# Kernel optimization log

Measured on AMD Instinct MI355X. Metric: run time of the kernel, lower is better.

Reference implementation:

```python
import jax, jax.numpy as jnp
import numpy as np

# module hyperparameters (init kwargs)
D_MODEL = 1024
NUM_HEADS = 16
D_K = D_MODEL // NUM_HEADS
WINDOW_SIZE = 256
GLOBAL_TOKENS = 64
SEQ_LEN = 4096
BATCH = 1
NEG_INF = float('-inf')


def build_local_window_mask(seq_len, window_size, global_tokens):
    # 0 where attention is allowed, -inf where blocked
    i = jnp.arange(seq_len)[:, None]
    j = jnp.arange(seq_len)[None, :]
    allowed = (i < global_tokens) | (j < global_tokens) | (jnp.abs(i - j) <= window_size)
    return jnp.where(allowed, 0.0, NEG_INF).astype(jnp.float32)


def setup_inputs() -> dict:
    key = jax.random.key(0)
    ks = jax.random.split(key, 12)
    s = 1.0 / np.sqrt(D_MODEL)
    inp = {
        'q': jax.random.normal(ks[0], (BATCH, SEQ_LEN, D_MODEL), jnp.float32),
        'k': jax.random.normal(ks[1], (BATCH, SEQ_LEN, D_MODEL), jnp.float32),
        'v': jax.random.normal(ks[2], (BATCH, SEQ_LEN, D_MODEL), jnp.float32),
        # nn.Linear weights: shape (out, in), applied as x @ W.T + b
        'w_q': jax.random.normal(ks[3], (D_MODEL, D_MODEL), jnp.float32) * s,
        'b_q': jax.random.normal(ks[4], (D_MODEL,), jnp.float32) * s,
        'w_k': jax.random.normal(ks[5], (D_MODEL, D_MODEL), jnp.float32) * s,
        'b_k': jax.random.normal(ks[6], (D_MODEL,), jnp.float32) * s,
        'w_v': jax.random.normal(ks[7], (D_MODEL, D_MODEL), jnp.float32) * s,
        'b_v': jax.random.normal(ks[8], (D_MODEL,), jnp.float32) * s,
        'w_o': jax.random.normal(ks[9], (D_MODEL, D_MODEL), jnp.float32) * s,
        'b_o': jax.random.normal(ks[10], (D_MODEL,), jnp.float32) * s,
    }
    return inp


def reference(q, k, v, w_q, b_q, w_k, b_k, w_v, b_v, w_o, b_o):
    B, S, _ = q.shape
    scale = 1.0 / np.sqrt(D_K)

    def proj(x, w, b):  # (B,S,D) -> (B,H,S,Dk)
        y = x @ w.T + b
        return y.reshape(B, S, NUM_HEADS, D_K).transpose(0, 2, 1, 3)

    Q = proj(q, w_q, b_q)
    K = proj(k, w_k, b_k)
    V = proj(v, w_v, b_v)

    local_mask = build_local_window_mask(S, WINDOW_SIZE, GLOBAL_TOKENS)  # (S,S)
    scores = jnp.einsum('bhqd,bhkd->bhqk', Q, K) * scale + local_mask[None, None]
    attn = jax.nn.softmax(scores, axis=-1)
    out = jnp.einsum('bhqk,bhkd->bhqd', attn, V)  # (B,H,S,Dk)
    out = out.transpose(0, 2, 1, 3).reshape(B, S, D_MODEL)
    return out @ w_o.T + b_o
```

## Files before the change

### kernel.cpp

```cpp
#include <hip/hip_runtime.h>

#define S_LEN 4096
#define DMODEL 1024
#define NHEADS 16
#define DKH 64
#define WIN 256
#define GTOK 64
#define NSPLIT 8

typedef unsigned short u16t;
typedef __attribute__((ext_vector_type(8))) short short8;
typedef __attribute__((ext_vector_type(4))) float f32x4;

__device__ __forceinline__ u16t f2bf(float x) {
  union { float f; unsigned int u; } v; v.f = x;
  unsigned int r = v.u + 0x7FFFu + ((v.u >> 16) & 1u);
  return (u16t)(r >> 16);
}

__device__ __forceinline__ unsigned int cvtpk(float lo, float hi) {
  unsigned int r;
  asm("v_cvt_pk_bf16_f32 %0, %1, %2" : "=v"(r) : "v"(lo), "v"(hi));
  return r;
}

__device__ __forceinline__ void gload_lds16(const u16t* g, u16t* l) {
  __builtin_amdgcn_global_load_lds(
      (const __attribute__((address_space(1))) void*)g,
      (__attribute__((address_space(3))) void*)l, 16, 0, 0);
}

__global__ void cvt_all(const float* __restrict__ s0, const float* __restrict__ s1,
                        const float* __restrict__ s2, const float* __restrict__ s3,
                        const float* __restrict__ s4, const float* __restrict__ s5,
                        const float* __restrict__ s6,
                        u16t* __restrict__ d0, u16t* __restrict__ d1,
                        u16t* __restrict__ d2, u16t* __restrict__ d3,
                        u16t* __restrict__ d4, u16t* __restrict__ d5,
                        u16t* __restrict__ d6) {
  size_t i = (size_t)blockIdx.x * 1024 + threadIdx.x * 4;
  const float* s; u16t* d; size_t local;
  if (i < ((size_t)4 << 20)) {
    int which = (int)(i >> 20);
    local = i & ((1u << 20) - 1);
    s = which == 0 ? s0 : which == 1 ? s1 : which == 2 ? s2 : s3;
    d = which == 0 ? d0 : which == 1 ? d1 : which == 2 ? d2 : d3;
  } else {
    size_t j = i - ((size_t)4 << 20);
    int which = (int)(j >> 22);
    local = j & ((1u << 22) - 1);
    s = which == 0 ? s4 : which == 1 ? s5 : s6;
    d = which == 0 ? d4 : which == 1 ? d5 : d6;
  }
  float4 f = *(const float4*)(s + local);
  unsigned int lo = (unsigned int)f2bf(f.x) | ((unsigned int)f2bf(f.y) << 16);
  unsigned int hi = (unsigned int)f2bf(f.z) | ((unsigned int)f2bf(f.w) << 16);
  *(uint2*)(d + local) = make_uint2(lo, hi);
}

#define BN 128
#define GBK 64

template<int OUT_F32, int BMT, int BIAS_ROW>
__device__ __forceinline__
void gemm_body(u16t* __restrict__ sA, u16t* __restrict__ sB,
               const u16t* __restrict__ A, const u16t* __restrict__ B,
               const float* __restrict__ bias, void* __restrict__ Y,
               int N, int K, float alpha, int m0, int n0)
{
  constexpr int MF = BMT / 32;
  constexpr int CA_ISS = BMT * 2 / 64;

  const int tid = threadIdx.x;
  const int lane = tid & 63;
  const int lr = lane & 15, lg = lane >> 4;
  const int w = tid >> 6;
  const int wm = (w >> 1) * (MF * 16), wn = (w & 1) * 64;

  f32x4 acc[MF][4] = {};
  const int nk = K / GBK;

  for (int kt = 0; kt < nk; ++kt) {
    if (kt) __syncthreads();
#pragma unroll
    for (int i = 0; i < CA_ISS; ++i) {
      int c0 = w * (BMT * 2) + i * 64;
      int c = c0 + lane;
      int row = c >> 3, g = (c & 7) ^ (row & 7);
      gload_lds16(A + (size_t)(m0 + row) * K + kt * GBK + g * 8, sA + (size_t)c0 * 8);
    }
#pragma unroll
    for (int i = 0; i < 4; ++i) {
      int c0 = w * 256 + i * 64;
      int c = c0 + lane;
      int row = c >> 3, g = (c & 7) ^ (row & 7);
      gload_lds16(B + (size_t)(n0 + row) * K + kt * GBK + g * 8, sB + (size_t)c0 * 8);
    }
    __syncthreads();

    short8 af[MF][2], bf[4][2];
#pragma unroll
    for (int mf = 0; mf < MF; ++mf)
#pragma unroll
      for (int kk = 0; kk < 2; ++kk) {
        int s = ((kk * 4 + lg) ^ (lr & 7));
        af[mf][kk] = *(const short8*)&sA[(wm + mf * 16 + lr) * GBK + s * 8];
      }
#pragma unroll
    for (int nf = 0; nf < 4; ++nf)
#pragma unroll
      for (int kk = 0; kk < 2; ++kk) {
        int s = ((kk * 4 + lg) ^ (lr & 7));
        bf[nf][kk] = *(const short8*)&sB[(wn + nf * 16 + lr) * GBK + s * 8];
      }
    __builtin_amdgcn_s_setprio(1);
#pragma unroll
    for (int kk = 0; kk < 2; ++kk)
#pragma unroll
      for (int mf = 0; mf < MF; ++mf)
#pragma unroll
        for (int nf = 0; nf < 4; ++nf)
          acc[mf][nf] = __builtin_amdgcn_mfma_f32_16x16x32_bf16(af[mf][kk], bf[nf][kk], acc[mf][nf], 0, 0, 0);
    __builtin_amdgcn_s_setprio(0);
  }

#pragma unroll
  for (int nf = 0; nf < 4; ++nf) {
    int col = n0 + wn + nf * 16 + lr;
    float bvc = BIAS_ROW ? 0.f : bias[col];
#pragma unroll
    for (int mf = 0; mf < MF; ++mf)
#pragma unroll
      for (int r = 0; r < 4; ++r) {
        int row = m0 + wm + mf * 16 + lg * 4 + r;
        float bv = BIAS_ROW ? bias[row] : bvc;
        float v = (acc[mf][nf][r] + bv) * alpha;
        if (OUT_F32) ((float*)Y)[(size_t)row * N + col] = v;
        else         ((u16t*)Y)[(size_t)row * N + col] = f2bf(v);
      }
  }
}

#define QSCALE 0.18033688011112042f
__global__ __launch_bounds__(256)
void gemm_qkv(const u16t* __restrict__ xq, const u16t* __restrict__ xk, const u16t* __restrict__ xv,
              const u16t* __restrict__ wq, const u16t* __restrict__ wk, const u16t* __restrict__ wv,
              const float* __restrict__ bq, const float* __restrict__ bk, const float* __restrict__ bv,
              u16t* __restrict__ Qp, u16t* __restrict__ Kp, u16t* __restrict__ Vt)
{
  __shared__ __align__(16) u16t smem[2 * 128 * GBK];
  u16t* sA = smem;
  u16t* sB = smem + 128 * GBK;

  int b = blockIdx.x;
  int wid = (b & 7) * 96 + (b >> 3);
  int z = wid >> 8;
  int rem = wid & 255;
  if (z == 0) {
    gemm_body<0, 128, 0>(sA, sB, xq, wq, bq, Qp, DMODEL, DMODEL, QSCALE, (rem >> 3) * 128, (rem & 7) * BN);
  } else if (z == 1) {
    gemm_body<0, 128, 0>(sA, sB, xk, wk, bk, Kp, DMODEL, DMODEL, 1.0f, (rem >> 3) * 128, (rem & 7) * BN);
  } else {
    gemm_body<0, 128, 1>(sA, sB, wv, xv, bv, Vt, S_LEN, DMODEL, 1.0f, (rem & 7) * 128, (rem >> 3) * BN);
  }
}

__global__ __launch_bounds__(256)
void gemm_o(const u16t* __restrict__ A, const u16t* __restrict__ B,
            const float* __restrict__ bias, float* __restrict__ Y)
{
  __shared__ __align__(16) u16t smem[(64 + 128) * GBK];
  u16t* sA = smem;
  u16t* sB = smem + 64 * GBK;

  int b = blockIdx.x;
  int wid = (b & 7) * 64 + (b >> 3);
  int my = wid >> 3, mx = wid & 7;
  gemm_body<1, 64, 0>(sA, sB, A, B, bias, Y, DMODEL, DMODEL, 1.0f, my * 64, mx * BN);
}

__global__ __launch_bounds__(256)
void attn_kernel(const u16t* __restrict__ Qp, const u16t* __restrict__ Kp,
                 const u16t* __restrict__ Vt, u16t* __restrict__ AO,
                 float* __restrict__ pacc, float* __restrict__ pml)
{
  __shared__ __align__(16) u16t sK[2][64 * 64];
  __shared__ __align__(16) u16t sV[2][64 * 64];
  __shared__ __align__(16) u16t sP[4][16 * 64];

  const int b = blockIdx.x;
  const int wid = (b & 7) * 142 + (b >> 3);
  const int h = wid / 71;
  const int x = wid % 71;

  const int tid = threadIdx.x, w = tid >> 6, lane = tid & 63;
  const int lr = lane & 15, lg = lane >> 4;

  const bool windowed = (x < 63);
  const int qb = windowed ? (x + 1) : 0;
  const int split = windowed ? 0 : (x - 63);
  const int qw = qb * 64 + w * 16;

  short8 qf[2];
#pragma unroll
  for (int kk = 0; kk < 2; ++kk)
    qf[kk] = *(const short8*)(Qp + (size_t)(qw + lr) * DMODEL + h * DKH + kk * 32 + lg * 8);

  f32x4 acc[4] = {};
  float m_run = -1e30f, l_run = 0.f;

  int lo = 1, nkv;
  if (windowed) {
    lo = (qb - 4 < 1) ? 1 : qb - 4;
    int hi = (qb + 4 > 63) ? 63 : qb + 4;
    nkv = hi - lo + 2;
  } else {
    nkv = 64 / NSPLIT;
  }

#define KVB(idx) (windowed ? ((idx) == 0 ? 0 : lo + (idx) - 1) : (split * (64 / NSPLIT) + (idx)))

  auto stage = [&](int buf, int kvb) {
    int kv0 = kvb * 64;
#pragma unroll
    for (int j = 0; j < 2; ++j) {
      int c = tid + j * 256;
      int row = c >> 3, g = (c & 7) ^ (row & 7);
      gload_lds16(Kp + (size_t)(kv0 + row) * DMODEL + h * DKH + g * 8, &sK[buf][c * 8]);
    }
#pragma unroll
    for (int j = 0; j < 2; ++j) {
      int c = tid + j * 256;
      int row = c >> 3, g = (c & 7) ^ (row & 7);
      gload_lds16(Vt + (size_t)(h * DKH + row) * S_LEN + kv0 + g * 8, &sV[buf][c * 8]);
    }
  };

  stage(0, KVB(0));
  __syncthreads();

  for (int idx = 0; idx < nkv; ++idx) {
    const int buf = idx & 1;
    const int kvb = KVB(idx);
    const int kv0 = kvb * 64;

    if (idx + 1 < nkv) stage(buf ^ 1, KVB(idx + 1));

    f32x4 sacc[4] = {};
    __builtin_amdgcn_s_setprio(1);
#pragma unroll
    for (int kk = 0; kk < 2; ++kk)
#pragma unroll
      for (int nf = 0; nf < 4; ++nf) {
        int s = ((kk * 4 + lg) ^ (lr & 7));
        short8 kf = *(const short8*)&sK[buf][(nf * 16 + lr) * 64 + s * 8];
        sacc[nf] = __builtin_amdgcn_mfma_f32_16x16x32_bf16(kf, qf[kk], sacc[nf], 0, 0, 0);
      }
    __builtin_amdgcn_s_setprio(0);

    if (windowed && (kvb == qb + 4 || (kvb == qb - 4 && kvb > 0))) {
      int qg = qw + lr;
#pragma unroll
      for (int nf = 0; nf < 4; ++nf)
#pragma unroll
        for (int r = 0; r < 4; ++r) {
          int sg = kv0 + nf * 16 + lg * 4 + r;
          int diff = qg - sg; if (diff < 0) diff = -diff;
          if (diff > WIN) sacc[nf][r] = -1e30f;
        }
    }

    float rm0 = fmaxf(fmaxf(sacc[0][0], sacc[0][1]), sacc[0][2]);
    float rm1 = fmaxf(fmaxf(sacc[0][3], sacc[1][0]), sacc[1][1]);
    float rm2 = fmaxf(fmaxf(sacc[1][2], sacc[1][3]), sacc[2][0]);
    float rm3 = fmaxf(fmaxf(sacc[2][1], sacc[2][2]), sacc[2][3]);
    float rm4 = fmaxf(fmaxf(sacc[3][0], sacc[3][1]), sacc[3][2]);
    float rm = fmaxf(fmaxf(rm0, rm1), fmaxf(fmaxf(rm2, rm3), fmaxf(rm4, sacc[3][3])));
    rm = fmaxf(rm, __shfl_xor(rm, 16));
    rm = fmaxf(rm, __shfl_xor(rm, 32));

    if (!__all(rm <= m_run + 11.0f)) {
      float mnew = fmaxf(m_run, rm);
      float corr = exp2f(m_run - mnew);
      m_run = mnew;
      l_run *= corr;
      float cq[4];
#pragma unroll
      for (int r = 0; r < 4; ++r) cq[r] = __shfl(corr, lg * 4 + r);
#pragma unroll
      for (int nf = 0; nf < 4; ++nf)
#pragma unroll
        for (int r = 0; r < 4; ++r) acc[nf][r] *= cq[r];
    }

    float p[4][4];
    float rs = 0.f;
#pragma unroll
    for (int nf = 0; nf < 4; ++nf)
#pragma unroll
      for (int r = 0; r < 4; ++r) {
        float e = exp2f(sacc[nf][r] - m_run);
        p[nf][r] = e;
        rs += e;
      }
    rs += __shfl_xor(rs, 16);
    rs += __shfl_xor(rs, 32);
    l_run += rs;

#pragma unroll
    for (int nf = 0; nf < 4; ++nf) {
      unsigned int lo32 = cvtpk(p[nf][0], p[nf][1]);
      unsigned int hi32 = cvtpk(p[nf][2], p[nf][3]);
      int blk = (nf * 2 + (lg >> 1)) ^ (lr & 7);
      *(uint2*)&sP[w][lr * 64 + blk * 8 + (lg & 1) * 4] = make_uint2(lo32, hi32);
    }

#pragma unroll
    for (int kk = 0; kk < 2; ++kk) {
      short8 pf = *(const short8*)&sP[w][lr * 64 + (((kk * 4 + lg) ^ (lr & 7))) * 8];
      __builtin_amdgcn_s_setprio(1);
#pragma unroll
      for (int nf = 0; nf < 4; ++nf) {
        int s = ((kk * 4 + lg) ^ (lr & 7));
        short8 vf = *(const short8*)&sV[buf][(nf * 16 + lr) * 64 + s * 8];
        acc[nf] = __builtin_amdgcn_mfma_f32_16x16x32_bf16(pf, vf, acc[nf], 0, 0, 0);
      }
      __builtin_amdgcn_s_setprio(0);
    }

    if (idx + 1 < nkv) __syncthreads();
  }
#undef KVB

  if (windowed) {
    float lq[4];
#pragma unroll
    for (int r = 0; r < 4; ++r) lq[r] = __shfl(l_run, lg * 4 + r);
#pragma unroll
    for (int nf = 0; nf < 4; ++nf)
#pragma unroll
      for (int r = 0; r < 4; ++r) {
        float v = acc[nf][r] / lq[r];
        AO[(size_t)(qw + lg * 4 + r) * DMODEL + h * DKH + nf * 16 + lr] = f2bf(v);
      }
  } else {
    const int pbase = (h * NSPLIT + split) * 64;
#pragma unroll
    for (int nf = 0; nf < 4; ++nf)
#pragma unroll
      for (int r = 0; r < 4; ++r)
        pacc[(size_t)(pbase + w * 16 + lg * 4 + r) * 64 + nf * 16 + lr] = acc[nf][r];
    if (lane < 16) {
      int bb = (pbase + w * 16 + lane) * 2;
      pml[bb] = m_run;
      pml[bb + 1] = l_run;
    }
  }
}

__global__ __launch_bounds__(256)
void merge_kernel(const float* __restrict__ pacc, const float* __restrict__ pml,
                  u16t* __restrict__ AO)
{
  const int h = blockIdx.x;
  const int tid = threadIdx.x;
  const int row = tid >> 2;
  const int d0 = (tid & 3) * 16;

  float M = -1e30f;
#pragma unroll
  for (int s = 0; s < NSPLIT; ++s)
    M = fmaxf(M, pml[((h * NSPLIT + s) * 64 + row) * 2]);

  float L = 0.f;
  float o[16];
#pragma unroll
  for (int e = 0; e < 16; ++e) o[e] = 0.f;

#pragma unroll
  for (int s = 0; s < NSPLIT; ++s) {
    int b = ((h * NSPLIT + s) * 64 + row) * 2;
    float sc = exp2f(pml[b] - M);
    L += pml[b + 1] * sc;
    const float4* a = (const float4*)(pacc + ((size_t)(h * NSPLIT + s) * 64 + row) * 64 + d0);
#pragma unroll
    for (int q4 = 0; q4 < 4; ++q4) {
      float4 av = a[q4];
      o[q4 * 4 + 0] += av.x * sc;
      o[q4 * 4 + 1] += av.y * sc;
      o[q4 * 4 + 2] += av.z * sc;
      o[q4 * 4 + 3] += av.w * sc;
    }
  }
  float inv = 1.f / L;
#pragma unroll
  for (int e = 0; e < 16; ++e)
    AO[(size_t)row * DMODEL + h * DKH + d0 + e] = f2bf(o[e] * inv);
}

extern "C" void kernel_launch(void* const* d_in, const int* in_sizes, int n_in,
                              void* d_out, int out_size, void* d_ws, size_t ws_size,
                              hipStream_t stream) {
  const float* q   = (const float*)d_in[0];
  const float* k   = (const float*)d_in[1];
  const float* v   = (const float*)d_in[2];
  const float* w_q = (const float*)d_in[3];
  const float* b_q = (const float*)d_in[4];
  const float* w_k = (const float*)d_in[5];
  const float* b_k = (const float*)d_in[6];
  const float* w_v = (const float*)d_in[7];
  const float* b_v = (const float*)d_in[8];
  const float* w_o = (const float*)d_in[9];
  const float* b_o = (const float*)d_in[10];

  u16t* ws = (u16t*)d_ws;
  const size_t SZX = (size_t)S_LEN * DMODEL;
  const size_t SZW = (size_t)DMODEL * DMODEL;
  u16t* xq  = ws;
  u16t* xk  = xq + SZX;
  u16t* xv  = xk + SZX;
  u16t* wb0 = xv + SZX;
  u16t* wb1 = wb0 + SZW;
  u16t* wb2 = wb1 + SZW;
  u16t* wb3 = wb2 + SZW;
  u16t* Qp  = wb3 + SZW;
  u16t* Kp  = Qp + SZX;
  u16t* Vt  = Kp + SZX;
  u16t* AO  = xk;
  float* pacc = (float*)xq;
  float* pml  = pacc + (size_t)NHEADS * NSPLIT * 64 * 64;

  dim3 blk(256);

  cvt_all<<<(int)((4 * SZW + 3 * SZX) / 1024), blk, 0, stream>>>(
      w_q, w_k, w_v, w_o, q, k, v, wb0, wb1, wb2, wb3, xq, xk, xv);

  gemm_qkv<<<768, blk, 0, stream>>>(xq, xk, xv, wb0, wb1, wb2, b_q, b_k, b_v, Qp, Kp, Vt);

  attn_kernel<<<(63 + NSPLIT) * NHEADS, blk, 0, stream>>>(Qp, Kp, Vt, AO, pacc, pml);
  merge_kernel<<<NHEADS, blk, 0, stream>>>(pacc, pml, AO);

  gemm_o<<<512, blk, 0, stream>>>(AO, wb3, b_o, (float*)d_out);
}
```

Baseline: 113.8 us.

## Load K/V fragments directly from global memory into registers in attention

Removes the double-buffered LDS staging of K and V tiles and the per-iteration block barriers. Each wave now loads its own MFMA K and V operand fragments straight from global memory into registers. This drops LDS traffic and synchronisation, but all four waves in a block now fetch the same K/V data redundantly. Load latency is also no longer hidden by prefetching the next tile, so it relies on L2/cache hits and on occupancy.

```diff
diff --git a/kernel.cpp b/kernel.cpp
--- a/kernel.cpp
+++ b/kernel.cpp
@@ -184,8 +184,6 @@
                  const u16t* __restrict__ Vt, u16t* __restrict__ AO,
                  float* __restrict__ pacc, float* __restrict__ pml)
 {
-  __shared__ __align__(16) u16t sK[2][64 * 64];
-  __shared__ __align__(16) u16t sV[2][64 * 64];
   __shared__ __align__(16) u16t sP[4][16 * 64];
 
   const int b = blockIdx.x;
@@ -218,45 +216,41 @@
     nkv = 64 / NSPLIT;
   }
 
+  const u16t* Kl = Kp + h * DKH + (size_t)lr * DMODEL + lg * 8;
+  const u16t* Vl = Vt + (size_t)(h * DKH + lr) * S_LEN + lg * 8;
+
 #define KVB(idx) (windowed ? ((idx) == 0 ? 0 : lo + (idx) - 1) : (split * (64 / NSPLIT) + (idx)))
 
-  auto stage = [&](int buf, int kvb) {
-    int kv0 = kvb * 64;
-#pragma unroll
-    for (int j = 0; j < 2; ++j) {
-      int c = tid + j * 256;
-      int row = c >> 3, g = (c & 7) ^ (row & 7);
-      gload_lds16(Kp + (size_t)(kv0 + row) * DMODEL + h * DKH + g * 8, &sK[buf][c * 8]);
-    }
-#pragma unroll
-    for (int j = 0; j < 2; ++j) {
-      int c = tid + j * 256;
-      int row = c >> 3, g = (c & 7) ^ (row & 7);
-      gload_lds16(Vt + (size_t)(h * DKH + row) * S_LEN + kv0 + g * 8, &sV[buf][c * 8]);
-    }
-  };
-
-  stage(0, KVB(0));
-  __syncthreads();
-
   for (int idx = 0; idx < nkv; ++idx) {
-    const int buf = idx & 1;
     const int kvb = KVB(idx);
     const int kv0 = kvb * 64;
 
-    if (idx + 1 < nkv) stage(buf ^ 1, KVB(idx + 1));
+    short8 kf[4][2];
+#pragma unroll
+    for (int nf = 0; nf < 4; ++nf) {
+      const u16t* kr = Kl + (size_t)(kv0 + nf * 16) * DMODEL;
+#pragma unroll
+      for (int kk = 0; kk < 2; ++kk)
+        kf[nf][kk] = *(const short8*)(kr + kk * 32);
+    }
 
     f32x4 sacc[4] = {};
     __builtin_amdgcn_s_setprio(1);
 #pragma unroll
     for (int kk = 0; kk < 2; ++kk)
 #pragma unroll
-      for (int nf = 0; nf < 4; ++nf) {
-        int s = ((kk * 4 + lg) ^ (lr & 7));
-        short8 kf = *(const short8*)&sK[buf][(nf * 16 + lr) * 64 + s * 8];
-        sacc[nf] = __builtin_amdgcn_mfma_f32_16x16x32_bf16(kf, qf[kk], sacc[nf], 0, 0, 0);
-      }
+      for (int nf = 0; nf < 4; ++nf)
+        sacc[nf] = __builtin_amdgcn_mfma_f32_16x16x32_bf16(kf[nf][kk], qf[kk], sacc[nf], 0, 0, 0);
     __builtin_amdgcn_s_setprio(0);
+
+    short8 vf[4][2];
+#pragma unroll
+    for (int nf = 0; nf < 4; ++nf) {
+      const u16t* vr = Vl + (size_t)(nf * 16) * S_LEN + kv0;
+#pragma unroll
+      for (int kk = 0; kk < 2; ++kk)
+        vf[nf][kk] = *(const short8*)(vr + kk * 32);
+    }
 
     if (windowed && (kvb == qb + 4 || (kvb == qb - 4 && kvb > 0))) {
       int qg = qw + lr;
@@ -320,15 +314,10 @@
       short8 pf = *(const short8*)&sP[w][lr * 64 + (((kk * 4 + lg) ^ (lr & 7))) * 8];
       __builtin_amdgcn_s_setprio(1);
 #pragma unroll
-      for (int nf = 0; nf < 4; ++nf) {
-        int s = ((kk * 4 + lg) ^ (lr & 7));
-        short8 vf = *(const short8*)&sV[buf][(nf * 16 + lr) * 64 + s * 8];
-        acc[nf] = __builtin_amdgcn_mfma_f32_16x16x32_bf16(pf, vf, acc[nf], 0, 0, 0);
-      }
+      for (int nf = 0; nf < 4; ++nf)
+        acc[nf] = __builtin_amdgcn_mfma_f32_16x16x32_bf16(pf, vf[nf][kk], acc[nf], 0, 0, 0);
       __builtin_amdgcn_s_setprio(0);
     }
-
-    if (idx + 1 < nkv) __syncthreads();
   }
 #undef KVB
 
```

After: 173.7 us. 1.53x slower.
